# Kernel optimization log

Measured on AMD Instinct MI355X. Metric: run time of the kernel, lower is better.

Reference implementation:

```python
import jax, jax.numpy as jnp
import numpy as np

N = 50000   # num_nodes
E = 1600000 # edges (avg degree 32)
D = 256     # in_feats
H = 256     # n_hidden


def setup_inputs() -> dict:
    key = jax.random.key(0)
    ks = jax.random.split(key, 9)
    s = 1.0 / np.sqrt(D)
    return {
        "input_nodes": jnp.arange(N, dtype=jnp.int32),
        "edge_src": jax.random.randint(ks[0], (E,), 0, N, dtype=jnp.int32),
        "edge_dst": jax.random.randint(ks[1], (E,), 0, N, dtype=jnp.int32),
        "emb": jax.random.normal(ks[2], (N, D), jnp.float32) * 0.02,
        "W_self0": jax.random.normal(ks[3], (D, H), jnp.float32) * s,
        "W_neigh0": jax.random.normal(ks[4], (D, H), jnp.float32) * s,
        "b0": jnp.zeros((H,), jnp.float32),
        "W_self1": jax.random.normal(ks[5], (H, H), jnp.float32) * s,
        "W_neigh1": jax.random.normal(ks[6], (H, H), jnp.float32) * s,
        "b1": jnp.zeros((H,), jnp.float32),
    }


def _sage_mean(h, src, dst, W_self, W_neigh, b, n):
    # gather neighbor features, mean-reduce by destination, then linear.
    msgs = h[src]                                                  # [E, d]
    ssum = jax.ops.segment_sum(msgs, dst, num_segments=n)          # [n, d]
    deg = jax.ops.segment_sum(jnp.ones(src.shape, h.dtype), dst, num_segments=n)
    h_neigh = ssum / jnp.maximum(deg, 1.0)[:, None]
    return h @ W_self + h_neigh @ W_neigh + b


def reference(input_nodes, edge_src, edge_dst, emb,
              W_self0, W_neigh0, b0, W_self1, W_neigh1, b1):
    h = emb[input_nodes]                                            # [N, D]
    h = _sage_mean(h, edge_src, edge_dst, W_self0, W_neigh0, b0, N)
    h = jax.nn.relu(h)  # dropout is identity at inference
    h = _sage_mean(h, edge_src, edge_dst, W_self1, W_neigh1, b1, N)
    h = h / jnp.linalg.norm(h)  # global Frobenius norm, as in torch.norm(h)
    return h
```

## Files before the change

kernel.cpp:

```cpp
#include <hip/hip_runtime.h>
#include <math.h>

#define NN 50000
#define NE 1600000
#define DF 256
#define NBUCK 391

typedef unsigned short ushortT;
typedef __attribute__((ext_vector_type(8))) short short8;
typedef __attribute__((ext_vector_type(4))) float floatx4;

__device__ __forceinline__ unsigned bf16rne(float f) {
    unsigned u = __float_as_uint(f);
    return (u + 0x7fffu + ((u >> 16) & 1u)) >> 16;
}

#define ASYNC16(gptr, ldsptr) \
    __builtin_amdgcn_global_load_lds((const __attribute__((address_space(1))) unsigned*)(gptr), \
                                     (__attribute__((address_space(3))) unsigned*)(ldsptr), 16, 0, 0)


__global__ void k_zero(int* __restrict__ bcnt) {
    int i = blockIdx.x * 256 + threadIdx.x;
    if (i < NBUCK) bcnt[i] = 0;
}

__global__ __launch_bounds__(256)
void k_bhist(const int* __restrict__ dst, int* __restrict__ bcnt) {
    __shared__ int h[NBUCK];
    for (int i = threadIdx.x; i < NBUCK; i += 256) h[i] = 0;
    __syncthreads();
    int base = blockIdx.x * 4096;
#pragma unroll
    for (int i = 0; i < 16; ++i) {
        int e = base + i * 256 + threadIdx.x;
        if (e < NE) atomicAdd(&h[dst[e] >> 7], 1);
    }
    __syncthreads();
    for (int i = threadIdx.x; i < NBUCK; i += 256)
        if (h[i]) atomicAdd(&bcnt[i], h[i]);
}

__global__ void k_bscan(const int* __restrict__ bcnt, int* __restrict__ bbase,
                        int* __restrict__ cursor, int* __restrict__ row_ptr,
                        float* __restrict__ nrm) {
    __shared__ int s[512];
    int t = threadIdx.x;
    int v = (t < NBUCK) ? bcnt[t] : 0;
    s[t] = v; __syncthreads();
    for (int off = 1; off < 512; off <<= 1) {
        int x = (t >= off) ? s[t - off] : 0;
        __syncthreads();
        s[t] += x;
        __syncthreads();
    }
    if (t < NBUCK) { bbase[t] = s[t] - v; cursor[t] = s[t] - v; }
    if (t == 0) { bbase[NBUCK] = NE; row_ptr[NN] = NE; *nrm = 0.0f; }
}

__global__ __launch_bounds__(256)
void k_bin(const int* __restrict__ src, const int* __restrict__ dst,
           int* __restrict__ cursor, unsigned* __restrict__ rec) {
    __shared__ int h[NBUCK];
    __shared__ int gb[NBUCK];
    for (int i = threadIdx.x; i < NBUCK; i += 256) h[i] = 0;
    __syncthreads();
    const int base = blockIdx.x * 2048;
    int bk[8], rk[8];
    unsigned pk[8];
#pragma unroll
    for (int i = 0; i < 8; ++i) {
        int e = base + i * 256 + threadIdx.x;
        if (e < NE) {
            int d = dst[e];
            bk[i] = d >> 7;
            pk[i] = (unsigned)src[e] | ((unsigned)(d & 127) << 16);
            rk[i] = atomicAdd(&h[bk[i]], 1);
        } else bk[i] = -1;
    }
    __syncthreads();
    for (int i = threadIdx.x; i < NBUCK; i += 256) {
        int c = h[i];
        gb[i] = c ? atomicAdd(&cursor[i], c) : 0;
    }
    __syncthreads();
#pragma unroll
    for (int i = 0; i < 8; ++i)
        if (bk[i] >= 0) rec[gb[bk[i]] + rk[i]] = pk[i];
}

__global__ __launch_bounds__(256)
void k_csr(const unsigned* __restrict__ rec, const int* __restrict__ bbase,
           int* __restrict__ row_ptr, ushortT* __restrict__ csr) {
    __shared__ int cnt[128];
    __shared__ int cur[128];
    __shared__ int s[256];
    const int B = blockIdx.x, t = threadIdx.x;
    if (t < 128) cnt[t] = 0;
    __syncthreads();
    const int beg = bbase[B], end = bbase[B + 1];
    for (int p = beg + t; p < end; p += 256)
        atomicAdd(&cnt[(rec[p] >> 16) & 127], 1);
    __syncthreads();
    int v = (t < 128) ? cnt[t] : 0;
    s[t] = v; __syncthreads();
    for (int off = 1; off < 256; off <<= 1) {
        int x = (t >= off) ? s[t - off] : 0;
        __syncthreads();
        s[t] += x;
        __syncthreads();
    }
    if (t < 128) {
        int ex = s[t] - v;
        cur[t] = ex;
        int node = B * 128 + t;
        if (node < NN) row_ptr[node] = beg + ex;
    }
    __syncthreads();
    for (int p = beg + t; p < end; p += 256) {
        unsigned r = rec[p];
        int loc = atomicAdd(&cur[(r >> 16) & 127], 1);
        csr[beg + loc] = (ushortT)r;
    }
}


__global__ __launch_bounds__(256)
void k_cvt_emb(const float* __restrict__ emb, const int* __restrict__ gather,
               ushortT* __restrict__ out) {
    long long i = ((long long)blockIdx.x * 256 + threadIdx.x) * 8;
    int row = (int)(i >> 8);
    int col = (int)(i & 255);
    long long g = (long long)gather[row] * 256 + col;
    float4 v0 = *(const float4*)(emb + g);
    float4 v1 = *(const float4*)(emb + g + 4);
    uint4 o;
    o.x = bf16rne(v0.x) | (bf16rne(v0.y) << 16);
    o.y = bf16rne(v0.z) | (bf16rne(v0.w) << 16);
    o.z = bf16rne(v1.x) | (bf16rne(v1.y) << 16);
    o.w = bf16rne(v1.z) | (bf16rne(v1.w) << 16);
    *(uint4*)(out + i) = o;
}

__global__ __launch_bounds__(256)
void k_cvt_w(const float* __restrict__ Ws, const float* __restrict__ Wn,
             ushortT* __restrict__ Wt) {
    int idx = blockIdx.x * 256 + threadIdx.x;
    int n = idx >> 9;
    int k = idx & 511;
    float v = (k < 256) ? Ws[k * 256 + n] : Wn[(k - 256) * 256 + n];
    Wt[idx] = (ushortT)bf16rne(v);
}


__global__ __launch_bounds__(256)
void k_agg(const ushortT* __restrict__ feat, const int* __restrict__ row_ptr,
           const ushortT* __restrict__ csr, ushortT* __restrict__ out) {
    int node = blockIdx.x * 4 + (threadIdx.x >> 6);
    int lane = threadIdx.x & 63;
    int half = lane >> 5;
    int l5 = lane & 31;
    if (node >= NN) return;
    int beg = row_ptr[node], end = row_ptr[node + 1];

    float s[8] = {0.f, 0.f, 0.f, 0.f, 0.f, 0.f, 0.f, 0.f};
    int p = beg + half;

#define ACCUM(q) do { \
        s[0] += __uint_as_float(q.x << 16); \
        s[1] += __uint_as_float(q.x & 0xffff0000u); \
        s[2] += __uint_as_float(q.y << 16); \
        s[3] += __uint_as_float(q.y & 0xffff0000u); \
        s[4] += __uint_as_float(q.z << 16); \
        s[5] += __uint_as_float(q.z & 0xffff0000u); \
        s[6] += __uint_as_float(q.w << 16); \
        s[7] += __uint_as_float(q.w & 0xffff0000u); \
    } while (0)

    for (; p + 14 < end; p += 16) {
        uint4 q[8];
#pragma unroll
        for (int i = 0; i < 8; ++i) {
            long long r = (long long)csr[p + 2 * i] * 256 + l5 * 8;
            q[i] = *(const uint4*)(feat + r);
        }
#pragma unroll
        for (int i = 0; i < 8; ++i) ACCUM(q[i]);
    }
    for (; p + 6 < end; p += 8) {
        uint4 q[4];
#pragma unroll
        for (int i = 0; i < 4; ++i) {
            long long r = (long long)csr[p + 2 * i] * 256 + l5 * 8;
            q[i] = *(const uint4*)(feat + r);
        }
#pragma unroll
        for (int i = 0; i < 4; ++i) ACCUM(q[i]);
    }
    for (; p < end; p += 2) {
        long long r0 = (long long)csr[p] * 256 + l5 * 8;
        uint4 a = *(const uint4*)(feat + r0);
        ACCUM(a);
    }
#undef ACCUM

#pragma unroll
    for (int k = 0; k < 8; ++k) s[k] += __shfl_down(s[k], 32);

    if (half == 0) {
        float inv = 1.0f / fmaxf((float)(end - beg), 1.0f);
        uint4 o;
        o.x = bf16rne(s[0] * inv) | (bf16rne(s[1] * inv) << 16);
        o.y = bf16rne(s[2] * inv) | (bf16rne(s[3] * inv) << 16);
        o.z = bf16rne(s[4] * inv) | (bf16rne(s[5] * inv) << 16);
        o.w = bf16rne(s[6] * inv) | (bf16rne(s[7] * inv) << 16);
        *(uint4*)(out + (long long)node * 256 + l5 * 8) = o;
    }
}


template<int RELU, int NORM>
__global__ __launch_bounds__(256, 3)
void k_gemm(const ushortT* __restrict__ Aself, const ushortT* __restrict__ Aneigh,
            const ushortT* __restrict__ Wt, const float* __restrict__ bias,
            ushortT* __restrict__ Cb, float* __restrict__ Cf, float* __restrict__ norm_acc) {
    __shared__ ushortT As[4096];
    __shared__ ushortT Bs[4096];
    __shared__ float red[4];

    const int t = threadIdx.x;
    const int w = t >> 6;
    const int lane = t & 63;
    const int m0 = blockIdx.x * 128;
    const int n0 = blockIdx.y * 128;

    const int r0 = t >> 2;
    const int cu = (t & 3) * 8;

    const long long gA0 = (long long)min(m0 + r0, NN - 1) * 256;
    const long long gA1 = (long long)min(m0 + r0 + 64, NN - 1) * 256;
    const long long gB0 = (long long)(n0 + r0) * 512;
    const long long gB1 = (long long)(n0 + r0 + 64) * 512;

    const unsigned lds0 = w * 512;
    const unsigned lds1 = 2048 + w * 512;

    const int wm = w & 1, wn = w >> 1;
    const int fm = lane & 15;
    const int fk = (lane >> 4) * 8;

    floatx4 acc[4][4];
#pragma unroll
    for (int i = 0; i < 4; ++i)
#pragma unroll
        for (int j = 0; j < 4; ++j) acc[i][j] = (floatx4){0.f, 0.f, 0.f, 0.f};

    for (int kt = 0; kt < 512; kt += 32) {
        const ushortT* Ab; int kc;
        if (kt < 256) { Ab = Aself; kc = kt; } else { Ab = Aneigh; kc = kt - 256; }

        __syncthreads();
        ASYNC16(Ab + gA0 + kc + cu, As + lds0);
        ASYNC16(Ab + gA1 + kc + cu, As + lds1);
        ASYNC16(Wt + gB0 + kt + cu, Bs + lds0);
        ASYNC16(Wt + gB1 + kt + cu, Bs + lds1);
        __syncthreads();

        short8 af[4], bf[4];
#pragma unroll
        for (int i = 0; i < 4; ++i)
            af[i] = *(const short8*)&As[(wm * 64 + i * 16 + fm) * 32 + fk];
#pragma unroll
        for (int j = 0; j < 4; ++j)
            bf[j] = *(const short8*)&Bs[(wn * 64 + j * 16 + fm) * 32 + fk];
#pragma unroll
        for (int i = 0; i < 4; ++i)
#pragma unroll
            for (int j = 0; j < 4; ++j)
                acc[i][j] = __builtin_amdgcn_mfma_f32_16x16x32_bf16(af[i], bf[j], acc[i][j], 0, 0, 0);
    }

    float bj[4];
#pragma unroll
    for (int j = 0; j < 4; ++j) bj[j] = bias[n0 + wn * 64 + j * 16 + fm];

    float sumsq = 0.0f;
#pragma unroll
    for (int i = 0; i < 4; ++i) {
#pragma unroll
        for (int r = 0; r < 4; ++r) {
            const int row = m0 + wm * 64 + i * 16 + (lane >> 4) * 4 + r;
            if (row < NN) {
#pragma unroll
                for (int j = 0; j < 4; ++j) {
                    const int col = n0 + wn * 64 + j * 16 + fm;
                    float v = acc[i][j][r] + bj[j];
                    if (RELU) v = fmaxf(v, 0.0f);
                    if (NORM) {
                        Cf[(long long)row * 256 + col] = v;
                        sumsq += v * v;
                    } else {
                        Cb[(long long)row * 256 + col] = (ushortT)bf16rne(v);
                    }
                }
            }
        }
    }

    if (NORM) {
#pragma unroll
        for (int off = 32; off > 0; off >>= 1) sumsq += __shfl_down(sumsq, off);
        if (lane == 0) red[w] = sumsq;
        __syncthreads();
        if (t == 0) atomicAdd(norm_acc, red[0] + red[1] + red[2] + red[3]);
    }
}

__global__ void k_scale(float* __restrict__ out, const float* __restrict__ nrm) {
    const float s = 1.0f / sqrtf(*nrm);
    long long i = ((long long)blockIdx.x * 256 + threadIdx.x) * 4;
    float4 v = *(float4*)&out[i];
    v.x *= s; v.y *= s; v.z *= s; v.w *= s;
    *(float4*)&out[i] = v;
}


extern "C" void kernel_launch(void* const* d_in, const int* in_sizes, int n_in,
                              void* d_out, int out_size, void* d_ws, size_t ws_size,
                              hipStream_t stream) {
    const int*   input_nodes = (const int*)d_in[0];
    const int*   esrc = (const int*)d_in[1];
    const int*   edst = (const int*)d_in[2];
    const float* emb  = (const float*)d_in[3];
    const float* Ws0  = (const float*)d_in[4];
    const float* Wn0  = (const float*)d_in[5];
    const float* b0   = (const float*)d_in[6];
    const float* Ws1  = (const float*)d_in[7];
    const float* Wn1  = (const float*)d_in[8];
    const float* b1   = (const float*)d_in[9];
    float* out = (float*)d_out;

    char* base = (char*)d_ws;
    ushortT*  embb    = (ushortT*) (base);
    ushortT*  h1b     = (ushortT*) (base + 25600000);
    ushortT*  hnb     = (ushortT*) (base + 51200000);
    unsigned* rec     = (unsigned*)(base + 76800000);
    ushortT*  csr     = (ushortT*) (base + 83200000);
    ushortT*  Wt0     = (ushortT*) (base + 86400000);
    ushortT*  Wt1     = (ushortT*) (base + 86662144);
    int*      row_ptr = (int*)     (base + 86924288);
    int*      bcnt    = (int*)     (base + 87124304);
    int*      bbase   = (int*)     (base + 87125904);
    int*      cursor  = (int*)     (base + 87127504);
    float*    nrm     = (float*)   (base + 87129104);

    k_zero  <<<2,     256, 0, stream>>>(bcnt);
    k_bhist <<<391,   256, 0, stream>>>(edst, bcnt);
    k_bscan <<<1,     512, 0, stream>>>(bcnt, bbase, cursor, row_ptr, nrm);
    k_bin   <<<782,   256, 0, stream>>>(esrc, edst, cursor, rec);
    k_csr   <<<NBUCK, 256, 0, stream>>>(rec, bbase, row_ptr, csr);

    k_cvt_emb<<<NN * DF / 8 / 256, 256, 0, stream>>>(emb, input_nodes, embb);
    k_cvt_w  <<<512, 256, 0, stream>>>(Ws0, Wn0, Wt0);
    k_cvt_w  <<<512, 256, 0, stream>>>(Ws1, Wn1, Wt1);

    dim3 gg((NN + 127) / 128, 2);

    k_agg<<<NN / 4, 256, 0, stream>>>(embb, row_ptr, csr, hnb);
    k_gemm<1, 0><<<gg, 256, 0, stream>>>(embb, hnb, Wt0, b0, h1b, nullptr, nullptr);

    k_agg<<<NN / 4, 256, 0, stream>>>(h1b, row_ptr, csr, hnb);
    k_gemm<0, 1><<<gg, 256, 0, stream>>>(h1b, hnb, Wt1, b1, nullptr, out, nrm);

    k_scale<<<NN * DF / 4 / 256, 256, 0, stream>>>(out, nrm);
}
```

Before: 478.5 us.

## Split aggregation over feature slices with eight edges per wave

The neighbor-mean aggregation is restructured so each block handles one 32-column feature slice (8 slices) for four nodes. Each wave processes 8 edges in parallel with 8-byte loads per lane instead of 2 edges with 16-byte loads. A three-step shuffle reduction replaces the single shuffle, and results go out through nontemporal stores. The aim is more memory-level parallelism and better L2 locality per slice. The cost is 8x more blocks, the csr indices being re-read once per slice, and smaller per-lane loads.

```diff
diff --git a/kernel.cpp b/kernel.cpp
--- a/kernel.cpp
+++ b/kernel.cpp
@@ -156,65 +156,57 @@
 __global__ __launch_bounds__(256)
 void k_agg(const ushortT* __restrict__ feat, const int* __restrict__ row_ptr,
            const ushortT* __restrict__ csr, ushortT* __restrict__ out) {
-    int node = blockIdx.x * 4 + (threadIdx.x >> 6);
-    int lane = threadIdx.x & 63;
-    int half = lane >> 5;
-    int l5 = lane & 31;
-    if (node >= NN) return;
-    int beg = row_ptr[node], end = row_ptr[node + 1];
-
-    float s[8] = {0.f, 0.f, 0.f, 0.f, 0.f, 0.f, 0.f, 0.f};
-    int p = beg + half;
-
-#define ACCUM(q) do { \
-        s[0] += __uint_as_float(q.x << 16); \
-        s[1] += __uint_as_float(q.x & 0xffff0000u); \
-        s[2] += __uint_as_float(q.y << 16); \
-        s[3] += __uint_as_float(q.y & 0xffff0000u); \
-        s[4] += __uint_as_float(q.z << 16); \
-        s[5] += __uint_as_float(q.z & 0xffff0000u); \
-        s[6] += __uint_as_float(q.w << 16); \
-        s[7] += __uint_as_float(q.w & 0xffff0000u); \
+    const int s = blockIdx.x & 7;
+    const int node = (blockIdx.x >> 3) * 4 + (threadIdx.x >> 6);
+    const int lane = threadIdx.x & 63;
+    const int es = lane >> 3;
+    const int cbase = s * 32 + (lane & 7) * 4;
+
+    const int beg = row_ptr[node], end = row_ptr[node + 1];
+    float a0 = 0.f, a1 = 0.f, a2 = 0.f, a3 = 0.f;
+
+#define ACC8(q) do { \
+        a0 += __uint_as_float(q.x << 16); \
+        a1 += __uint_as_float(q.x & 0xffff0000u); \
+        a2 += __uint_as_float(q.y << 16); \
+        a3 += __uint_as_float(q.y & 0xffff0000u); \
     } while (0)
 
-    for (; p + 14 < end; p += 16) {
-        uint4 q[8];
-#pragma unroll
-        for (int i = 0; i < 8; ++i) {
-            long long r = (long long)csr[p + 2 * i] * 256 + l5 * 8;
-            q[i] = *(const uint4*)(feat + r);
-        }
-#pragma unroll
-        for (int i = 0; i < 8; ++i) ACCUM(q[i]);
-    }
-    for (; p + 6 < end; p += 8) {
-        uint4 q[4];
-#pragma unroll
-        for (int i = 0; i < 4; ++i) {
-            long long r = (long long)csr[p + 2 * i] * 256 + l5 * 8;
-            q[i] = *(const uint4*)(feat + r);
-        }
-#pragma unroll
-        for (int i = 0; i < 4; ++i) ACCUM(q[i]);
-    }
-    for (; p < end; p += 2) {
-        long long r0 = (long long)csr[p] * 256 + l5 * 8;
-        uint4 a = *(const uint4*)(feat + r0);
-        ACCUM(a);
-    }
-#undef ACCUM
-
-#pragma unroll
-    for (int k = 0; k < 8; ++k) s[k] += __shfl_down(s[k], 32);
-
-    if (half == 0) {
-        float inv = 1.0f / fmaxf((float)(end - beg), 1.0f);
-        uint4 o;
-        o.x = bf16rne(s[0] * inv) | (bf16rne(s[1] * inv) << 16);
-        o.y = bf16rne(s[2] * inv) | (bf16rne(s[3] * inv) << 16);
-        o.z = bf16rne(s[4] * inv) | (bf16rne(s[5] * inv) << 16);
-        o.w = bf16rne(s[6] * inv) | (bf16rne(s[7] * inv) << 16);
-        *(uint4*)(out + (long long)node * 256 + l5 * 8) = o;
+    int p = beg;
+    for (; p + 16 <= end; p += 16) {
+        const int r0 = (int)csr[p + es] * DF + cbase;
+        const int r1 = (int)csr[p + 8 + es] * DF + cbase;
+        const uint2 q0 = *(const uint2*)(feat + r0);
+        const uint2 q1 = *(const uint2*)(feat + r1);
+        ACC8(q0); ACC8(q1);
+    }
+    if (p + 8 <= end) {
+        const int r0 = (int)csr[p + es] * DF + cbase;
+        const uint2 q0 = *(const uint2*)(feat + r0);
+        ACC8(q0);
+        p += 8;
+    }
+    const int rem = end - p;
+    if (es < rem) {
+        const int r0 = (int)csr[p + es] * DF + cbase;
+        const uint2 q0 = *(const uint2*)(feat + r0);
+        ACC8(q0);
+    }
+#undef ACC8
+
+    a0 += __shfl_down(a0, 32); a1 += __shfl_down(a1, 32);
+    a2 += __shfl_down(a2, 32); a3 += __shfl_down(a3, 32);
+    a0 += __shfl_down(a0, 16); a1 += __shfl_down(a1, 16);
+    a2 += __shfl_down(a2, 16); a3 += __shfl_down(a3, 16);
+    a0 += __shfl_down(a0, 8);  a1 += __shfl_down(a1, 8);
+    a2 += __shfl_down(a2, 8);  a3 += __shfl_down(a3, 8);
+
+    if (es == 0) {
+        const float inv = 1.0f / fmaxf((float)(end - beg), 1.0f);
+        const unsigned lo = bf16rne(a0 * inv) | (bf16rne(a1 * inv) << 16);
+        const unsigned hi = bf16rne(a2 * inv) | (bf16rne(a3 * inv) << 16);
+        const unsigned long long v = (unsigned long long)lo | ((unsigned long long)hi << 32);
+        __builtin_nontemporal_store(v, (unsigned long long*)(out + (long long)node * DF + cbase));
     }
 }
 
@@ -365,11 +357,12 @@
     k_cvt_w  <<<512, 256, 0, stream>>>(Ws1, Wn1, Wt1);
 
     dim3 gg((NN + 127) / 128, 2);
-
-    k_agg<<<NN / 4, 256, 0, stream>>>(embb, row_ptr, csr, hnb);
+    const int AGG_BLOCKS = (NN / 4) * 8;
+
+    k_agg<<<AGG_BLOCKS, 256, 0, stream>>>(embb, row_ptr, csr, hnb);
     k_gemm<1, 0><<<gg, 256, 0, stream>>>(embb, hnb, Wt0, b0, h1b, nullptr, nullptr);
 
-    k_agg<<<NN / 4, 256, 0, stream>>>(h1b, row_ptr, csr, hnb);
+    k_agg<<<AGG_BLOCKS, 256, 0, stream>>>(h1b, row_ptr, csr, hnb);
     k_gemm<0, 1><<<gg, 256, 0, stream>>>(h1b, hnb, Wt1, b1, nullptr, out, nrm);
 
     k_scale<<<NN * DF / 4 / 256, 256, 0, stream>>>(out, nrm);
```

After: 594.2 us. 1.24x slower.
